# Kernel optimization log

Hardware: AMD Instinct MI355X
Metric: run time of the kernel (lower is better)

## Reference

```python
import jax, jax.numpy as jnp
import numpy as np

N = 50000      # nodes
E = 600000     # edges
D = 128        # dim_h == num_features
G = 512        # graphs in batch
BN_EPS = 1e-5


def _w(k, shape, fan_in):
    return jax.random.normal(k, shape, jnp.float32) * np.float32(1.0 / np.sqrt(fan_in))


def setup_inputs() -> dict:
    key = jax.random.key(0)
    ks = jax.random.split(key, 16)
    return {
        "x": jax.random.normal(ks[0], (N, D), jnp.float32),
        "edge_index": jax.random.randint(ks[1], (2, E), 0, N, jnp.int64),
        "batch": jnp.sort(jax.random.randint(ks[2], (N,), 0, G, jnp.int64)),
        # GINConv 1 MLP: Linear -> BN -> ReLU -> Linear -> ReLU
        "c1_W1": _w(ks[3], (D, D), D), "c1_b1": jnp.zeros((D,), jnp.float32),
        "c1_g": jnp.ones((D,), jnp.float32), "c1_be": jnp.zeros((D,), jnp.float32),
        "c1_W2": _w(ks[4], (D, D), D), "c1_b2": jnp.zeros((D,), jnp.float32),
        # GINConv 2 MLP
        "c2_W1": _w(ks[5], (D, D), D), "c2_b1": jnp.zeros((D,), jnp.float32),
        "c2_g": jnp.ones((D,), jnp.float32), "c2_be": jnp.zeros((D,), jnp.float32),
        "c2_W2": _w(ks[6], (D, D), D), "c2_b2": jnp.zeros((D,), jnp.float32),
        # readout MLP
        "lin1_W": _w(ks[7], (4 * D, 4 * D), 4 * D), "lin1_b": jnp.zeros((4 * D,), jnp.float32),
        "lin2_W": _w(ks[8], (4 * D, 1), 4 * D), "lin2_b": jnp.zeros((1,), jnp.float32),
    }


def _gin_conv(x, src, dst, W1, b1, g, be, W2, b2):
    # sum aggregation of neighbor messages (PyG GINConv, eps=0)
    agg = jax.ops.segment_sum(x[src], dst, num_segments=x.shape[0])
    h = (agg + x) @ W1 + b1
    # BatchNorm1d, training mode (biased batch stats over nodes)
    mu = h.mean(axis=0)
    var = h.var(axis=0)
    h = jax.nn.relu(g * (h - mu) * jax.lax.rsqrt(var + BN_EPS) + be)
    return jax.nn.relu(h @ W2 + b2)


def _pool(h, batch):
    add = jax.ops.segment_sum(h, batch, num_segments=G)
    mx = jax.ops.segment_max(h, batch, num_segments=G)
    mx = jnp.where(jnp.isfinite(mx), mx, 0.0)  # empty segments -> 0
    return add, mx


def reference(x, edge_index, batch,
              c1_W1, c1_b1, c1_g, c1_be, c1_W2, c1_b2,
              c2_W1, c2_b1, c2_g, c2_be, c2_W2, c2_b2,
              lin1_W, lin1_b, lin2_W, lin2_b):
    src, dst = edge_index[0], edge_index[1]
    h1 = _gin_conv(x, src, dst, c1_W1, c1_b1, c1_g, c1_be, c1_W2, c1_b2)
    h2 = _gin_conv(h1, src, dst, c2_W1, c2_b1, c2_g, c2_be, c2_W2, c2_b2)
    a1, m1 = _pool(h1, batch)
    a2, m2 = _pool(h2, batch)
    h = jnp.concatenate([a1, a2, m1, m2], axis=1)  # [G, 4D]
    h = jax.nn.relu(h @ lin1_W + lin1_b)
    h = h @ lin2_W + lin2_b  # [G, 1]
    return jax.nn.sigmoid(h), h
```

## Files before the change

kernel.cpp:

```cpp
#include <hip/hip_runtime.h>

#define D 128
#define GNUM 512

typedef _Float16 f16;
typedef _Float16 f16x2 __attribute__((ext_vector_type(2)));
typedef _Float16 f16x8 __attribute__((ext_vector_type(8)));
typedef float f32x4 __attribute__((ext_vector_type(4)));

__global__ void deg_kernel(const int* __restrict__ ei, int* __restrict__ deg,
                           int nE) {
  int e = blockIdx.x * blockDim.x + threadIdx.x;
  if (e < nE) atomicAdd(&deg[ei[nE + e]], 1);
}

__global__ __launch_bounds__(256) void partial_kernel(
    const int* __restrict__ deg, int* __restrict__ partials, int n) {
  __shared__ int sh[256];
  const int t = threadIdx.x;
  const int i = blockIdx.x * 512 + t * 2;
  int s = 0;
  if (i < n) s += deg[i];
  if (i + 1 < n) s += deg[i + 1];
  sh[t] = s;
  __syncthreads();
#pragma unroll
  for (int off = 128; off > 0; off >>= 1) {
    if (t < off) sh[t] += sh[t + off];
    __syncthreads();
  }
  if (t == 0) partials[blockIdx.x] = sh[0];
}

__global__ __launch_bounds__(128) void scanp_kernel(
    int* __restrict__ partials, int nP, int* __restrict__ rowptr, int n,
    int nE) {
  __shared__ int sh[128];
  const int t = threadIdx.x;
  const int v = (t < nP) ? partials[t] : 0;
  sh[t] = v;
  __syncthreads();
#pragma unroll
  for (int off = 1; off < 128; off <<= 1) {
    int u = (t >= off) ? sh[t - off] : 0;
    __syncthreads();
    sh[t] += u;
    __syncthreads();
  }
  if (t < nP) partials[t] = sh[t] - v;
  if (t == 0) rowptr[n] = nE;
}

__global__ __launch_bounds__(256) void emit_kernel(
    const int* __restrict__ deg, const int* __restrict__ partials,
    int* __restrict__ rowptr, int* __restrict__ cursor, int n) {
  __shared__ int sh[256];
  const int t = threadIdx.x;
  const int i = blockIdx.x * 512 + t * 2;
  const int d0 = (i < n) ? deg[i] : 0;
  const int d1 = (i + 1 < n) ? deg[i + 1] : 0;
  const int s = d0 + d1;
  sh[t] = s;
  __syncthreads();
#pragma unroll
  for (int off = 1; off < 256; off <<= 1) {
    int u = (t >= off) ? sh[t - off] : 0;
    __syncthreads();
    sh[t] += u;
    __syncthreads();
  }
  int base = partials[blockIdx.x] + sh[t] - s;
  if (i < n) {
    rowptr[i] = base;
    cursor[i] = base;
    base += d0;
  }
  if (i + 1 < n) {
    rowptr[i + 1] = base;
    cursor[i + 1] = base;
  }
}

__global__ void fill_kernel(const int* __restrict__ ei, int* __restrict__ cursor,
                            int* __restrict__ csr, int nE) {
  int e = blockIdx.x * blockDim.x + threadIdx.x;
  if (e < nE) {
    int d = ei[nE + e];
    int pos = atomicAdd(&cursor[d], 1);
    csr[pos] = ei[e];
  }
}

__global__ void gstart_kernel(const int* __restrict__ batch,
                              int* __restrict__ gstart, int n) {
  int g = blockIdx.x * blockDim.x + threadIdx.x;
  if (g > GNUM) return;
  if (g == GNUM) { gstart[g] = n; return; }
  int lo = 0, hi = n;
  while (lo < hi) {
    int mid = (lo + hi) >> 1;
    if (batch[mid] < g) lo = mid + 1; else hi = mid;
  }
  gstart[g] = lo;
}

__global__ void xcvt_kernel(const float* __restrict__ in, f16* __restrict__ out,
                            int n4) {
  int i = blockIdx.x * 256 + threadIdx.x;
  if (i < n4) {
    float4 v = ((const float4*)in)[i];
    union { f16 h[4]; uint2 u; } p;
    p.h[0] = (f16)v.x; p.h[1] = (f16)v.y; p.h[2] = (f16)v.z; p.h[3] = (f16)v.w;
    ((uint2*)out)[i] = p.u;
  }
}

__global__ void wprep_kernel(const float* __restrict__ W0,
                             const float* __restrict__ W1,
                             const float* __restrict__ W2,
                             const float* __restrict__ W3,
                             f16* __restrict__ out) {
  int idx = blockIdx.x * 256 + threadIdx.x;
  int wsel = idx >> 14;
  int rem = idx & 16383;
  int col = rem >> 7, k = rem & 127;
  const float* W = (wsel == 0) ? W0 : (wsel == 1) ? W1 : (wsel == 2) ? W2 : W3;
  out[idx] = (f16)W[k * D + col];
}

__global__ __launch_bounds__(256) void aggw_kernel(
    const f16* __restrict__ feat, const int* __restrict__ rowptr,
    const int* __restrict__ csr, f16* __restrict__ out, int n) {
  const int row = blockIdx.x * 4 + (threadIdx.x >> 6);
  const int l = threadIdx.x & 63;
  if (row >= n) return;
  const int c = l * 2;
  float a0, a1;
  {
    f16x2 v = *(const f16x2*)(feat + (size_t)row * D + c);
    a0 = (float)v[0]; a1 = (float)v[1];
  }
  const int beg = rowptr[row], end = rowptr[row + 1];
  int i = beg;
  for (; i + 3 < end; i += 4) {
    int s0 = csr[i], s1 = csr[i + 1], s2 = csr[i + 2], s3 = csr[i + 3];
    f16x2 v0 = *(const f16x2*)(feat + (size_t)s0 * D + c);
    f16x2 v1 = *(const f16x2*)(feat + (size_t)s1 * D + c);
    f16x2 v2 = *(const f16x2*)(feat + (size_t)s2 * D + c);
    f16x2 v3 = *(const f16x2*)(feat + (size_t)s3 * D + c);
    a0 += (float)v0[0] + (float)v1[0] + (float)v2[0] + (float)v3[0];
    a1 += (float)v0[1] + (float)v1[1] + (float)v2[1] + (float)v3[1];
  }
  for (; i < end; i++) {
    f16x2 v = *(const f16x2*)(feat + (size_t)csr[i] * D + c);
    a0 += (float)v[0];
    a1 += (float)v[1];
  }
  f16x2 o;
  o[0] = (f16)a0;
  o[1] = (f16)a1;
  *(f16x2*)(out + (size_t)row * D + c) = o;
}

template <int BN, int OUT>
__global__ __launch_bounds__(64) void gemm16_kernel(
    const f16* __restrict__ A, const float* __restrict__ ss,
    const f16* __restrict__ WT, const float* __restrict__ bias,
    f16* __restrict__ C, float* __restrict__ pstat, int n) {
  const int l = threadIdx.x;
  const int rw0 = blockIdx.x * 32;
  const int lr = l & 15;
  const int lq = l >> 4;
  const int lk = lq * 8;

  f32x4 acc[2][8];
#pragma unroll
  for (int m = 0; m < 2; m++)
#pragma unroll
    for (int nt = 0; nt < 8; nt++) acc[m][nt] = (f32x4)0.f;

#pragma unroll
  for (int s = 0; s < 4; s++) {
    const int k = s * 32 + lk;
    f16x8 af[2];
#pragma unroll
    for (int m = 0; m < 2; m++) {
      int row = rw0 + m * 16 + lr;
      f16x8 v = (f16x8)(f16)0.f;
      if (row < n) v = *(const f16x8*)(A + (size_t)row * D + k);
      if (BN) {
        float4 c0 = *(const float4*)(ss + k);
        float4 c1 = *(const float4*)(ss + k + 4);
        float4 h0 = *(const float4*)(ss + 128 + k);
        float4 h1 = *(const float4*)(ss + 128 + k + 4);
        f16x8 r;
        r[0] = (f16)fmaxf(0.f, fmaf((float)v[0], c0.x, h0.x));
        r[1] = (f16)fmaxf(0.f, fmaf((float)v[1], c0.y, h0.y));
        r[2] = (f16)fmaxf(0.f, fmaf((float)v[2], c0.z, h0.z));
        r[3] = (f16)fmaxf(0.f, fmaf((float)v[3], c0.w, h0.w));
        r[4] = (f16)fmaxf(0.f, fmaf((float)v[4], c1.x, h1.x));
        r[5] = (f16)fmaxf(0.f, fmaf((float)v[5], c1.y, h1.y));
        r[6] = (f16)fmaxf(0.f, fmaf((float)v[6], c1.z, h1.z));
        r[7] = (f16)fmaxf(0.f, fmaf((float)v[7], c1.w, h1.w));
        af[m] = r;
      } else {
        af[m] = v;
      }
    }
    f16x8 bf[8];
#pragma unroll
    for (int nt = 0; nt < 8; nt++)
      bf[nt] = *(const f16x8*)(WT + (size_t)(nt * 16 + lr) * D + k);
#pragma unroll
    for (int m = 0; m < 2; m++)
#pragma unroll
      for (int nt = 0; nt < 8; nt++)
        acc[m][nt] = __builtin_amdgcn_mfma_f32_16x16x32_f16(af[m], bf[nt],
                                                            acc[m][nt], 0, 0, 0);
  }

  if constexpr (OUT == 0) {
    float ts[8], tq[8];
#pragma unroll
    for (int nt = 0; nt < 8; nt++) { ts[nt] = 0.f; tq[nt] = 0.f; }
#pragma unroll
    for (int m = 0; m < 2; m++)
#pragma unroll
      for (int r = 0; r < 4; r++) {
        int row = rw0 + m * 16 + lq * 4 + r;
        if (row < n) {
#pragma unroll
          for (int nt = 0; nt < 8; nt++) {
            float v = acc[m][nt][r] + bias[nt * 16 + lr];
            C[(size_t)row * D + nt * 16 + lr] = (f16)v;
            ts[nt] += v;
            tq[nt] = fmaf(v, v, tq[nt]);
          }
        }
      }
#pragma unroll
    for (int nt = 0; nt < 8; nt++) {
      ts[nt] += __shfl_xor(ts[nt], 16); ts[nt] += __shfl_xor(ts[nt], 32);
      tq[nt] += __shfl_xor(tq[nt], 16); tq[nt] += __shfl_xor(tq[nt], 32);
    }
    if (l < 16) {
      float* ps = pstat + (size_t)blockIdx.x * 256;
#pragma unroll
      for (int nt = 0; nt < 8; nt++) {
        ps[nt * 16 + l] = ts[nt];
        ps[128 + nt * 16 + l] = tq[nt];
      }
    }
  } else {
#pragma unroll
    for (int m = 0; m < 2; m++)
#pragma unroll
      for (int r = 0; r < 4; r++) {
        int row = rw0 + m * 16 + lq * 4 + r;
        if (row < n) {
#pragma unroll
          for (int nt = 0; nt < 8; nt++) {
            float v = fmaxf(0.f, acc[m][nt][r] + bias[nt * 16 + lr]);
            C[(size_t)row * D + nt * 16 + lr] = (f16)v;
          }
        }
      }
  }
}

__global__ __launch_bounds__(256) void statreduce_kernel(
    const float* __restrict__ pstat, float* __restrict__ pstat2, int nB) {
  int c = threadIdx.x;
  float s = 0.f;
  for (int b = blockIdx.x; b < nB; b += 32)
    s += pstat[(size_t)b * 256 + c];
  pstat2[(size_t)blockIdx.x * 256 + c] = s;
}

__global__ void bnstats_kernel(const float* __restrict__ pstat2,
                               const float* __restrict__ g,
                               const float* __restrict__ be,
                               float* __restrict__ ss, int n) {
  int c = threadIdx.x;
  float s = 0.f, sq = 0.f;
#pragma unroll
  for (int i = 0; i < 32; i++) {
    s += pstat2[i * 256 + c];
    sq += pstat2[i * 256 + 128 + c];
  }
  float inv_n = 1.0f / (float)n;
  float mean = s * inv_n;
  float var = sq * inv_n - mean * mean;
  float scale = g[c] * rsqrtf(var + 1e-5f);
  ss[c] = scale;
  ss[128 + c] = be[c] - mean * scale;
}

__global__ __launch_bounds__(256) void pool2_kernel(
    const f16* __restrict__ h1, const f16* __restrict__ h2,
    const int* __restrict__ gstart, float* __restrict__ pooled) {
  int g = blockIdx.x;
  int c = threadIdx.x & 127;
  int half = threadIdx.x >> 7;
  int r0 = gstart[g], r1 = gstart[g + 1];
  float s1 = 0.f, m1 = 0.f, s2 = 0.f, m2 = 0.f;
  for (int r = r0 + half; r < r1; r += 2) {
    float v1 = (float)h1[(size_t)r * D + c];
    float v2 = (float)h2[(size_t)r * D + c];
    s1 += v1; m1 = fmaxf(m1, v1);
    s2 += v2; m2 = fmaxf(m2, v2);
  }
  __shared__ float sh[256];
  sh[threadIdx.x] = s1; __syncthreads();
  if (half == 0) s1 += sh[threadIdx.x + 128];
  __syncthreads(); sh[threadIdx.x] = s2; __syncthreads();
  if (half == 0) s2 += sh[threadIdx.x + 128];
  __syncthreads(); sh[threadIdx.x] = m1; __syncthreads();
  if (half == 0) m1 = fmaxf(m1, sh[threadIdx.x + 128]);
  __syncthreads(); sh[threadIdx.x] = m2; __syncthreads();
  if (half == 0) {
    m2 = fmaxf(m2, sh[threadIdx.x + 128]);
    float* pg = pooled + (size_t)g * 512;
    pg[c] = s1;
    pg[128 + c] = s2;
    pg[256 + c] = m1;
    pg[384 + c] = m2;
  }
}

__global__ __launch_bounds__(512) void lin1_kernel(
    const float* __restrict__ pooled, const float* __restrict__ W,
    float* __restrict__ out1) {
  __shared__ float prow[4][128];
  const int j = threadIdx.x;
  const int gt = blockIdx.x >> 2;
  const int kt = blockIdx.x & 3;
  const int g0 = gt * 4, k0 = kt * 128;
  prow[j >> 7][j & 127] = pooled[(size_t)(g0 + (j >> 7)) * 512 + k0 + (j & 127)];
  __syncthreads();
  float acc[4] = {0.f, 0.f, 0.f, 0.f};
  for (int k = 0; k < 128; k++) {
    float w = W[(size_t)(k0 + k) * 512 + j];
#pragma unroll
    for (int r = 0; r < 4; r++) acc[r] = fmaf(prow[r][k], w, acc[r]);
  }
#pragma unroll
  for (int r = 0; r < 4; r++)
    atomicAdd(out1 + (size_t)(g0 + r) * 512 + j, acc[r]);
}

__global__ void lin2_kernel(const float* __restrict__ out1,
                            const float* __restrict__ b1,
                            const float* __restrict__ W,
                            const float* __restrict__ b2,
                            float* __restrict__ out) {
  int g = blockIdx.x;
  int lane = threadIdx.x;
  float s = 0.f;
  for (int k = lane; k < 512; k += 64)
    s = fmaf(fmaxf(0.f, out1[(size_t)g * 512 + k] + b1[k]), W[k], s);
#pragma unroll
  for (int off = 32; off > 0; off >>= 1) s += __shfl_down(s, off);
  if (lane == 0) {
    float h = s + b2[0];
    out[g] = 1.0f / (1.0f + expf(-h));
    out[GNUM + g] = h;
  }
}

extern "C" void kernel_launch(void* const* d_in, const int* in_sizes, int n_in,
                              void* d_out, int out_size, void* d_ws,
                              size_t ws_size, hipStream_t stream) {
  const float* x = (const float*)d_in[0];
  const int* ei = (const int*)d_in[1];
  const int* batch = (const int*)d_in[2];
  const float* c1_W1 = (const float*)d_in[3];
  const float* c1_b1 = (const float*)d_in[4];
  const float* c1_g  = (const float*)d_in[5];
  const float* c1_be = (const float*)d_in[6];
  const float* c1_W2 = (const float*)d_in[7];
  const float* c1_b2 = (const float*)d_in[8];
  const float* c2_W1 = (const float*)d_in[9];
  const float* c2_b1 = (const float*)d_in[10];
  const float* c2_g  = (const float*)d_in[11];
  const float* c2_be = (const float*)d_in[12];
  const float* c2_W2 = (const float*)d_in[13];
  const float* c2_b2 = (const float*)d_in[14];
  const float* lin1_W = (const float*)d_in[15];
  const float* lin1_b = (const float*)d_in[16];
  const float* lin2_W = (const float*)d_in[17];
  const float* lin2_b = (const float*)d_in[18];

  const int n = in_sizes[0] / D;
  const int nE = in_sizes[1] / 2;

  char* p = (char*)d_ws;
  auto take = [&](size_t bytes) {
    char* r = p;
    p += (bytes + 255) & ~(size_t)255;
    return r;
  };
  f16*   hpre   = (f16*)take((size_t)n * D * 2);
  f16*   aggt   = (f16*)take((size_t)n * D * 2);
  f16*   h1     = (f16*)take((size_t)n * D * 2);
  f16*   wt     = (f16*)take(4 * 16384 * 2);
  float* pooled = (float*)take((size_t)GNUM * 512 * 4);
  float* out1b  = (float*)take((size_t)GNUM * 512 * 4);
  int*   deg    = (int*)take((size_t)n * 4);
  float* ssbuf  = (float*)take(256 * 4);
  int*   gstart = (int*)take((GNUM + 1) * 4);
  int* rowptr   = (int*)take((size_t)(n + 1) * 4);
  int* cursor   = (int*)take((size_t)(n + 1) * 4);
  int* partials = (int*)take(128 * 4);
  int* csr      = (int*)take((size_t)nE * 4);
  const int nB = (n + 31) / 32;
  float* pstat  = (float*)take((size_t)nB * 256 * 4);
  float* pstat2 = (float*)take(32 * 256 * 4);

  const int edge_grid = (nE + 255) / 256;
  const int aggw_grid = (n + 3) / 4;
  const int nP = (n + 511) / 512;
  const int n4 = n * D / 4;

  hipMemsetAsync(out1b, 0, (size_t)GNUM * 512 * 4 + (size_t)n * 4, stream);
  deg_kernel<<<edge_grid, 256, 0, stream>>>(ei, deg, nE);
  partial_kernel<<<nP, 256, 0, stream>>>(deg, partials, n);
  scanp_kernel<<<1, 128, 0, stream>>>(partials, nP, rowptr, n, nE);
  emit_kernel<<<nP, 256, 0, stream>>>(deg, partials, rowptr, cursor, n);
  fill_kernel<<<edge_grid, 256, 0, stream>>>(ei, cursor, csr, nE);
  gstart_kernel<<<3, 256, 0, stream>>>(batch, gstart, n);
  wprep_kernel<<<256, 256, 0, stream>>>(c1_W1, c1_W2, c2_W1, c2_W2, wt);
  xcvt_kernel<<<(n4 + 255) / 256, 256, 0, stream>>>(x, h1, n4);

  aggw_kernel<<<aggw_grid, 256, 0, stream>>>(h1, rowptr, csr, aggt, n);
  gemm16_kernel<0, 0><<<nB, 64, 0, stream>>>(aggt, nullptr, wt, c1_b1, hpre,
                                             pstat, n);
  statreduce_kernel<<<32, 256, 0, stream>>>(pstat, pstat2, nB);
  bnstats_kernel<<<1, 128, 0, stream>>>(pstat2, c1_g, c1_be, ssbuf, n);
  gemm16_kernel<1, 1><<<nB, 64, 0, stream>>>(hpre, ssbuf, wt + 16384, c1_b2,
                                             h1, nullptr, n);

  aggw_kernel<<<aggw_grid, 256, 0, stream>>>(h1, rowptr, csr, aggt, n);
  gemm16_kernel<0, 0><<<nB, 64, 0, stream>>>(aggt, nullptr, wt + 32768, c2_b1,
                                             hpre, pstat, n);
  statreduce_kernel<<<32, 256, 0, stream>>>(pstat, pstat2, nB);
  bnstats_kernel<<<1, 128, 0, stream>>>(pstat2, c2_g, c2_be, ssbuf, n);
  gemm16_kernel<1, 1><<<nB, 64, 0, stream>>>(hpre, ssbuf, wt + 49152, c2_b2,
                                             aggt, nullptr, n);

  pool2_kernel<<<GNUM, 256, 0, stream>>>(h1, aggt, gstart, pooled);
  lin1_kernel<<<512, 512, 0, stream>>>(pooled, lin1_W, out1b);
  lin2_kernel<<<GNUM, 64, 0, stream>>>(out1b, lin1_b, lin2_W, lin2_b,
                                       (float*)d_out);
}
```

Measured before the change: 282.8 us.

## Fuse prep kernels and fuse pooling with readout MLP into one kernel

Merges the x conversion, weight transpose and graph-start search into a single launch using block-range dispatch. Also fuses pooling, lin1 (full K per block, no atomics) and lin2 into one kernel that processes 4 graphs per block, so the pooled and out1 buffers and their memset go away. This removes several launches and intermediate global traffic. In exchange the readout now runs only 128 blocks, each looping over all 512 K rows of lin1_W, which gives less parallelism than the previous 512-block split.

```diff
diff --git a/kernel.cpp b/kernel.cpp
--- a/kernel.cpp
+++ b/kernel.cpp
@@ -91,41 +91,41 @@
   }
 }
 
-__global__ void gstart_kernel(const int* __restrict__ batch,
-                              int* __restrict__ gstart, int n) {
-  int g = blockIdx.x * blockDim.x + threadIdx.x;
-  if (g > GNUM) return;
-  if (g == GNUM) { gstart[g] = n; return; }
-  int lo = 0, hi = n;
-  while (lo < hi) {
-    int mid = (lo + hi) >> 1;
-    if (batch[mid] < g) lo = mid + 1; else hi = mid;
-  }
-  gstart[g] = lo;
-}
-
-__global__ void xcvt_kernel(const float* __restrict__ in, f16* __restrict__ out,
-                            int n4) {
-  int i = blockIdx.x * 256 + threadIdx.x;
-  if (i < n4) {
-    float4 v = ((const float4*)in)[i];
-    union { f16 h[4]; uint2 u; } p;
-    p.h[0] = (f16)v.x; p.h[1] = (f16)v.y; p.h[2] = (f16)v.z; p.h[3] = (f16)v.w;
-    ((uint2*)out)[i] = p.u;
-  }
-}
-
-__global__ void wprep_kernel(const float* __restrict__ W0,
-                             const float* __restrict__ W1,
-                             const float* __restrict__ W2,
-                             const float* __restrict__ W3,
-                             f16* __restrict__ out) {
-  int idx = blockIdx.x * 256 + threadIdx.x;
-  int wsel = idx >> 14;
-  int rem = idx & 16383;
-  int col = rem >> 7, k = rem & 127;
-  const float* W = (wsel == 0) ? W0 : (wsel == 1) ? W1 : (wsel == 2) ? W2 : W3;
-  out[idx] = (f16)W[k * D + col];
+__global__ __launch_bounds__(256) void prep_kernel(
+    const float* __restrict__ x, f16* __restrict__ x16, int n4,
+    const float* __restrict__ W0, const float* __restrict__ W1,
+    const float* __restrict__ W2, const float* __restrict__ W3,
+    f16* __restrict__ wt, const int* __restrict__ batch,
+    int* __restrict__ gstart, int n, int nxblk) {
+  const int b = blockIdx.x;
+  if (b < nxblk) {
+    int i = b * 256 + threadIdx.x;
+    if (i < n4) {
+      float4 v = ((const float4*)x)[i];
+      union { f16 h[4]; uint2 u; } p;
+      p.h[0] = (f16)v.x; p.h[1] = (f16)v.y;
+      p.h[2] = (f16)v.z; p.h[3] = (f16)v.w;
+      ((uint2*)x16)[i] = p.u;
+    }
+  } else if (b < nxblk + 256) {
+    int idx = (b - nxblk) * 256 + threadIdx.x;
+    int wsel = idx >> 14;
+    int rem = idx & 16383;
+    int col = rem >> 7, k = rem & 127;
+    const float* W = (wsel == 0) ? W0 : (wsel == 1) ? W1
+                                      : (wsel == 2) ? W2 : W3;
+    wt[idx] = (f16)W[k * D + col];
+  } else {
+    int g = (b - nxblk - 256) * 256 + threadIdx.x;
+    if (g > GNUM) return;
+    if (g == GNUM) { gstart[g] = n; return; }
+    int lo = 0, hi = n;
+    while (lo < hi) {
+      int mid = (lo + hi) >> 1;
+      if (batch[mid] < g) lo = mid + 1; else hi = mid;
+    }
+    gstart[g] = lo;
+  }
 }
 
 __global__ __launch_bounds__(256) void aggw_kernel(
@@ -296,75 +296,70 @@
   ss[128 + c] = be[c] - mean * scale;
 }
 
-__global__ __launch_bounds__(256) void pool2_kernel(
+__global__ __launch_bounds__(512) void poolout_kernel(
     const f16* __restrict__ h1, const f16* __restrict__ h2,
-    const int* __restrict__ gstart, float* __restrict__ pooled) {
-  int g = blockIdx.x;
-  int c = threadIdx.x & 127;
-  int half = threadIdx.x >> 7;
-  int r0 = gstart[g], r1 = gstart[g + 1];
-  float s1 = 0.f, m1 = 0.f, s2 = 0.f, m2 = 0.f;
-  for (int r = r0 + half; r < r1; r += 2) {
-    float v1 = (float)h1[(size_t)r * D + c];
-    float v2 = (float)h2[(size_t)r * D + c];
-    s1 += v1; m1 = fmaxf(m1, v1);
-    s2 += v2; m2 = fmaxf(m2, v2);
-  }
-  __shared__ float sh[256];
-  sh[threadIdx.x] = s1; __syncthreads();
-  if (half == 0) s1 += sh[threadIdx.x + 128];
-  __syncthreads(); sh[threadIdx.x] = s2; __syncthreads();
-  if (half == 0) s2 += sh[threadIdx.x + 128];
-  __syncthreads(); sh[threadIdx.x] = m1; __syncthreads();
-  if (half == 0) m1 = fmaxf(m1, sh[threadIdx.x + 128]);
-  __syncthreads(); sh[threadIdx.x] = m2; __syncthreads();
-  if (half == 0) {
-    m2 = fmaxf(m2, sh[threadIdx.x + 128]);
-    float* pg = pooled + (size_t)g * 512;
-    pg[c] = s1;
-    pg[128 + c] = s2;
-    pg[256 + c] = m1;
-    pg[384 + c] = m2;
-  }
-}
-
-__global__ __launch_bounds__(512) void lin1_kernel(
-    const float* __restrict__ pooled, const float* __restrict__ W,
-    float* __restrict__ out1) {
-  __shared__ float prow[4][128];
-  const int j = threadIdx.x;
-  const int gt = blockIdx.x >> 2;
-  const int kt = blockIdx.x & 3;
-  const int g0 = gt * 4, k0 = kt * 128;
-  prow[j >> 7][j & 127] = pooled[(size_t)(g0 + (j >> 7)) * 512 + k0 + (j & 127)];
+    const int* __restrict__ gstart, const float* __restrict__ W1,
+    const float* __restrict__ b1, const float* __restrict__ W2,
+    const float* __restrict__ b2, float* __restrict__ out) {
+  __shared__ float prow[4][512];
+  __shared__ float shred[8][4];
+  const int t = threadIdx.x;
+  const int g0 = blockIdx.x * 4;
+  {
+    const int sub = t >> 7;
+    const int c = t & 127;
+    const int r0 = gstart[g0 + sub], r1 = gstart[g0 + sub + 1];
+    float s1 = 0.f, m1 = 0.f, s2 = 0.f, m2 = 0.f;
+    int r = r0;
+    for (; r + 1 < r1; r += 2) {
+      float a1 = (float)h1[(size_t)r * D + c];
+      float b1v = (float)h1[(size_t)(r + 1) * D + c];
+      float a2 = (float)h2[(size_t)r * D + c];
+      float b2v = (float)h2[(size_t)(r + 1) * D + c];
+      s1 += a1 + b1v; m1 = fmaxf(m1, fmaxf(a1, b1v));
+      s2 += a2 + b2v; m2 = fmaxf(m2, fmaxf(a2, b2v));
+    }
+    if (r < r1) {
+      float a1 = (float)h1[(size_t)r * D + c];
+      float a2 = (float)h2[(size_t)r * D + c];
+      s1 += a1; m1 = fmaxf(m1, a1);
+      s2 += a2; m2 = fmaxf(m2, a2);
+    }
+    prow[sub][c] = s1;
+    prow[sub][128 + c] = s2;
+    prow[sub][256 + c] = m1;
+    prow[sub][384 + c] = m2;
+  }
   __syncthreads();
   float acc[4] = {0.f, 0.f, 0.f, 0.f};
-  for (int k = 0; k < 128; k++) {
-    float w = W[(size_t)(k0 + k) * 512 + j];
+  for (int k = 0; k < 512; k++) {
+    float w = W1[(size_t)k * 512 + t];
 #pragma unroll
     for (int r = 0; r < 4; r++) acc[r] = fmaf(prow[r][k], w, acc[r]);
   }
+  const float bj = b1[t];
+  const float w2 = W2[t];
 #pragma unroll
   for (int r = 0; r < 4; r++)
-    atomicAdd(out1 + (size_t)(g0 + r) * 512 + j, acc[r]);
-}
-
-__global__ void lin2_kernel(const float* __restrict__ out1,
-                            const float* __restrict__ b1,
-                            const float* __restrict__ W,
-                            const float* __restrict__ b2,
-                            float* __restrict__ out) {
-  int g = blockIdx.x;
-  int lane = threadIdx.x;
-  float s = 0.f;
-  for (int k = lane; k < 512; k += 64)
-    s = fmaf(fmaxf(0.f, out1[(size_t)g * 512 + k] + b1[k]), W[k], s);
-#pragma unroll
-  for (int off = 32; off > 0; off >>= 1) s += __shfl_down(s, off);
-  if (lane == 0) {
+    acc[r] = fmaxf(0.f, acc[r] + bj) * w2;
+  const int w = t >> 6, l = t & 63;
+#pragma unroll
+  for (int r = 0; r < 4; r++) {
+#pragma unroll
+    for (int off = 32; off > 0; off >>= 1) acc[r] += __shfl_down(acc[r], off);
+  }
+  if (l == 0) {
+#pragma unroll
+    for (int r = 0; r < 4; r++) shred[w][r] = acc[r];
+  }
+  __syncthreads();
+  if (t < 4) {
+    float s = 0.f;
+#pragma unroll
+    for (int i = 0; i < 8; i++) s += shred[i][t];
     float h = s + b2[0];
-    out[g] = 1.0f / (1.0f + expf(-h));
-    out[GNUM + g] = h;
+    out[g0 + t] = 1.0f / (1.0f + expf(-h));
+    out[GNUM + g0 + t] = h;
   }
 }
 
@@ -404,8 +399,6 @@
   f16*   aggt   = (f16*)take((size_t)n * D * 2);
   f16*   h1     = (f16*)take((size_t)n * D * 2);
   f16*   wt     = (f16*)take(4 * 16384 * 2);
-  float* pooled = (float*)take((size_t)GNUM * 512 * 4);
-  float* out1b  = (float*)take((size_t)GNUM * 512 * 4);
   int*   deg    = (int*)take((size_t)n * 4);
   float* ssbuf  = (float*)take(256 * 4);
   int*   gstart = (int*)take((GNUM + 1) * 4);
@@ -421,16 +414,18 @@
   const int aggw_grid = (n + 3) / 4;
   const int nP = (n + 511) / 512;
   const int n4 = n * D / 4;
-
-  hipMemsetAsync(out1b, 0, (size_t)GNUM * 512 * 4 + (size_t)n * 4, stream);
+  const int nxblk = (n4 + 255) / 256;
+  const int prep_grid = nxblk + 256 + 3;
+
+  hipMemsetAsync(deg, 0, (size_t)n * sizeof(int), stream);
   deg_kernel<<<edge_grid, 256, 0, stream>>>(ei, deg, nE);
   partial_kernel<<<nP, 256, 0, stream>>>(deg, partials, n);
   scanp_kernel<<<1, 128, 0, stream>>>(partials, nP, rowptr, n, nE);
   emit_kernel<<<nP, 256, 0, stream>>>(deg, partials, rowptr, cursor, n);
   fill_kernel<<<edge_grid, 256, 0, stream>>>(ei, cursor, csr, nE);
-  gstart_kernel<<<3, 256, 0, stream>>>(batch, gstart, n);
-  wprep_kernel<<<256, 256, 0, stream>>>(c1_W1, c1_W2, c2_W1, c2_W2, wt);
-  xcvt_kernel<<<(n4 + 255) / 256, 256, 0, stream>>>(x, h1, n4);
+  prep_kernel<<<prep_grid, 256, 0, stream>>>(x, h1, n4, c1_W1, c1_W2, c2_W1,
+                                             c2_W2, wt, batch, gstart, n,
+                                             nxblk);
 
   aggw_kernel<<<aggw_grid, 256, 0, stream>>>(h1, rowptr, csr, aggt, n);
   gemm16_kernel<0, 0><<<nB, 64, 0, stream>>>(aggt, nullptr, wt, c1_b1, hpre,
@@ -448,8 +443,7 @@
   gemm16_kernel<1, 1><<<nB, 64, 0, stream>>>(hpre, ssbuf, wt + 49152, c2_b2,
                                              aggt, nullptr, n);
 
-  pool2_kernel<<<GNUM, 256, 0, stream>>>(h1, aggt, gstart, pooled);
-  lin1_kernel<<<512, 512, 0, stream>>>(pooled, lin1_W, out1b);
-  lin2_kernel<<<GNUM, 64, 0, stream>>>(out1b, lin1_b, lin2_W, lin2_b,
-                                       (float*)d_out);
-}
+  poolout_kernel<<<GNUM / 4, 512, 0, stream>>>(h1, aggt, gstart, lin1_W,
+                                               lin1_b, lin2_W, lin2_b,
+                                               (float*)d_out);
+}
```

New measurement: 282.5 us. Within noise of the previous version (-0.1%).
